# Optimization experiments

Measured on AMD Instinct MI355X. Metric: run time of the kernel, lower is better.

The kernel has to match this reference:

```python
import jax, jax.numpy as jnp
import numpy as np

B, L, A, DF = 8, 2048, 25, 128
T = 20  # amino-acid types
NUM_FUNCS = 3
D_IN = 2 * DF + T * A * 3 + 3 * (NUM_FUNCS * 4 + 1)  # 1795


def setup_inputs() -> dict:
    key = jax.random.key(0)
    ks = jax.random.split(key, 16)
    chain_emb = jax.random.normal(ks[7], (10, DF), dtype=jnp.float32)
    chain_emb = chain_emb.at[0].set(0.0)  # padding_idx=0
    return {
        'seq': jax.random.randint(ks[0], (B, L), 0, T),
        'xyz': jax.random.normal(ks[1], (B, L, A, 3), dtype=jnp.float32),
        'dihedrals': jax.random.normal(ks[2], (B, L, 3), dtype=jnp.float32),
        'chain_idx': jax.random.randint(ks[3], (B, L), 0, 10),
        'orientation': jax.random.normal(ks[4], (B, L, 3, 3), dtype=jnp.float32),
        'atom_mask': jnp.ones((B, L, A), dtype=jnp.float32),
        'aa_emb': jax.random.normal(ks[6], (T, DF), dtype=jnp.float32),
        'chain_emb': chain_emb,
        'W1': jax.random.normal(ks[8], (D_IN, 2 * DF), dtype=jnp.float32) * 0.02,
        'b1': jnp.zeros((2 * DF,), dtype=jnp.float32),
        'W2': jax.random.normal(ks[9], (2 * DF, DF), dtype=jnp.float32) * 0.05,
        'b2': jnp.zeros((DF,), dtype=jnp.float32),
        'W3': jax.random.normal(ks[10], (DF, DF), dtype=jnp.float32) * 0.05,
        'b3': jnp.zeros((DF,), dtype=jnp.float32),
        'W4': jax.random.normal(ks[11], (DF, DF), dtype=jnp.float32) * 0.05,
        'b4': jnp.zeros((DF,), dtype=jnp.float32),
    }


def _angular_encoding(x):
    # x: (..., d_in) -> (..., d_in * (num_funcs*4 + 1))
    freq = jnp.array([1.0, 2.0, 3.0, 1.0, 0.5, 1.0 / 3.0], dtype=x.dtype)
    xe = x[..., None]  # (..., d_in, 1)
    enc = jnp.concatenate([xe, jnp.sin(freq * xe), jnp.cos(freq * xe)], axis=-1)
    return enc.reshape(*x.shape[:-1], -1)


def reference(seq, xyz, dihedrals, chain_idx, orientation, atom_mask,
              aa_emb, chain_emb, W1, b1, W2, b2, W3, b3, W4, b4):
    b, l = seq.shape
    CA_IDX = 1
    aa_type_feat = aa_emb[seq]  # (b,l,DF)
    # local frame coords: R^T (x - x_CA) per atom
    xyz_rel = xyz - xyz[:, :, CA_IDX:CA_IDX + 1, :]
    xyz_local = jnp.einsum('blji,blaj->blai', orientation, xyz_rel)  # (b,l,A,3)
    # type-conditioned one-hot scatter of local coords -> (b,l,T*A*3)
    onehot = jax.nn.one_hot(seq, T, dtype=xyz.dtype)  # (b,l,T)
    coord_feat = jnp.einsum('blt,blad->bltad', onehot, xyz_local).reshape(b, l, -1)
    dihedral_feat = _angular_encoding(dihedrals)  # (b,l,39)
    chain_feat = jnp.where((chain_idx == 0)[..., None], 0.0, chain_emb[chain_idx])
    x = jnp.concatenate([aa_type_feat, coord_feat, dihedral_feat, chain_feat], axis=-1)
    h = jax.nn.relu(x @ W1 + b1)
    h = jax.nn.relu(h @ W2 + b2)
    h = jax.nn.relu(h @ W3 + b3)
    return h @ W4 + b4
```

## Files before the change

kernel.cpp:

```cpp
#include <hip/hip_runtime.h>

#define NRES   16384
#define NTYPES 20
#define CAP    1280
#define MT     32
#define CHUNKS 32
#define FPP    392
#define H1P    264
#define H2P    136


#define BUCKET_OFF  512
#define W1S_OFF     32768
#define W1C_OFF     110592
#define W2_OFF      520192
#define W3_OFF      552960
#define W4_OFF      569344

typedef __attribute__((ext_vector_type(8))) short short8;
typedef __attribute__((ext_vector_type(4))) float float4_;

__device__ __forceinline__ unsigned short f2bf(float f) {
    union { float f; unsigned int u; } v; v.f = f;
    unsigned int r = v.u + 0x7FFF + ((v.u >> 16) & 1);
    return (unsigned short)(r >> 16);
}

__global__ void zero_counts_k(int* __restrict__ cnt) {
    if (threadIdx.x < NTYPES) cnt[threadIdx.x] = 0;
}

__global__ void prep_k(const int* __restrict__ seq, int* __restrict__ cnt,
                       const float* __restrict__ W1, const float* __restrict__ W2,
                       const float* __restrict__ W3, const float* __restrict__ W4,
                       unsigned short* __restrict__ ws) {
    const int blk = blockIdx.x, tid = threadIdx.x;
    if (blk < 64) {
        __shared__ int lcnt[NTYPES], lbase[NTYPES];
        if (tid < NTYPES) lcnt[tid] = 0;
        __syncthreads();
        const int r = blk * 256 + tid;
        const int t = seq[r];
        const int sl = atomicAdd(&lcnt[t], 1);
        __syncthreads();
        if (tid < NTYPES && lcnt[tid] > 0)
            lbase[tid] = atomicAdd(&cnt[tid], lcnt[tid]);
        __syncthreads();
        const int slot = lbase[t] + sl;
        if (slot < CAP) ws[BUCKET_OFF + t * CAP + slot] = (unsigned short)r;
        return;
    }
    int i = (blk - 64) * 256 + tid;
    float v[8];
    int dst;
    if (i < 9728) {
        const int g = i >> 8, n = i & 255;
        const int s0 = g * 8;
#pragma unroll
        for (int j = 0; j < 8; ++j) {
            const int s = s0 + j;
            const int row = (s < 128) ? s : (s < 168 ? s + 1500 : s + 1499);
            v[j] = (s0 < 296) ? W1[(size_t)row * 256 + n] : 0.0f;
        }
        dst = W1S_OFF + (g * 256 + n) * 8;
    } else if ((i -= 9728) < 51200) {
        const int t = i / 2560, r2 = i - t * 2560;
        const int g = r2 >> 8, n = r2 & 255;
        const int c0 = g * 8;
#pragma unroll
        for (int j = 0; j < 8; ++j) {
            const int c = c0 + j;
            v[j] = (c < 75) ? W1[(size_t)(128 + 75 * t + c) * 256 + n] : 0.0f;
        }
        dst = W1C_OFF + ((t * 10 + g) * 256 + n) * 8;
    } else if ((i -= 51200) < 4096) {
        const int g = i >> 7, n = i & 127;
#pragma unroll
        for (int j = 0; j < 8; ++j) v[j] = W2[(size_t)(g * 8 + j) * 128 + n];
        dst = W2_OFF + (g * 128 + n) * 8;
    } else if ((i -= 4096) < 2048) {
        const int g = i >> 7, n = i & 127;
#pragma unroll
        for (int j = 0; j < 8; ++j) v[j] = W3[(size_t)(g * 8 + j) * 128 + n];
        dst = W3_OFF + (g * 128 + n) * 8;
    } else {
        i -= 2048;
        const int g = i >> 7, n = i & 127;
#pragma unroll
        for (int j = 0; j < 8; ++j) v[j] = W4[(size_t)(g * 8 + j) * 128 + n];
        dst = W4_OFF + (g * 128 + n) * 8;
    }
    short8 o;
#pragma unroll
    for (int j = 0; j < 8; ++j) o[j] = (short)f2bf(v[j]);
    *(short8*)(ws + dst) = o;
}

__global__ __launch_bounds__(512, 6) void residue_embed_k(
    const float* __restrict__ xyz, const float* __restrict__ dihedrals,
    const int* __restrict__ chain_idx, const float* __restrict__ orient,
    const float* __restrict__ aa_emb, const float* __restrict__ chain_emb,
    const float* __restrict__ b1, const float* __restrict__ b2,
    const float* __restrict__ b3, const float* __restrict__ b4,
    const unsigned short* __restrict__ ws, float* __restrict__ out)
{
    __shared__ __align__(16) unsigned short feat[MT * FPP];
    __shared__ __align__(16) unsigned short h1s[MT * H1P];
    __shared__ int ridx[MT];

    const int* cnt = (const int*)ws;
    const unsigned short* bucket = ws + BUCKET_OFF;

    const int t = blockIdx.x / CHUNKS;
    const int start = (blockIdx.x % CHUNKS) * MT;
    const int count = cnt[t];
    if (start >= count) return;
    const int mact = min(MT, count - start);
    const int tid = threadIdx.x;

    {
        const int m = tid >> 4, s = tid & 15;
        const int idx = bucket[t * CAP + min(start + m, count - 1)];
        if (s == 0) ridx[m] = idx;
        unsigned short* fm = &feat[m * FPP];
#pragma unroll
        for (int i = 0; i < 8; ++i) fm[s * 8 + i] = f2bf(aa_emb[t * 128 + s * 8 + i]);
        const int c = chain_idx[idx];
#pragma unroll
        for (int i = 0; i < 8; ++i)
            fm[248 + s * 8 + i] = f2bf((c == 0) ? 0.0f : chain_emb[c * 128 + s * 8 + i]);
        const float* xr = &xyz[(size_t)idx * 75];
        const float cax = xr[3], cay = xr[4], caz = xr[5];
        const float* R = &orient[(size_t)idx * 9];
        for (int a = s; a < 25; a += 16) {
            float rx = xr[a * 3] - cax, ry = xr[a * 3 + 1] - cay, rz = xr[a * 3 + 2] - caz;
#pragma unroll
            for (int i = 0; i < 3; ++i)
                fm[128 + a * 3 + i] = f2bf(R[i] * rx + R[3 + i] * ry + R[6 + i] * rz);
        }
        if (s < 13) {
            const int qd = (s == 0) ? 0 : (s < 7 ? s - 1 : s - 7);
            const float fq = (qd == 0) ? 1.f : (qd == 1) ? 2.f : (qd == 2) ? 3.f
                           : (qd == 3) ? 1.f : (qd == 4) ? 0.5f : (1.f / 3.f);
#pragma unroll
            for (int d = 0; d < 3; ++d) {
                float x = dihedrals[idx * 3 + d];
                float v = (s == 0) ? x : (s < 7 ? sinf(fq * x) : cosf(fq * x));
                fm[208 + d * 13 + s] = f2bf(v);
            }
        }
        if (s == 14) { for (int k = 203; k < 208; ++k) fm[k] = 0; }
        if (s == 13) fm[247] = 0;
        if (s == 12) { for (int k = 376; k < 384; ++k) fm[k] = 0; }
    }
    __syncthreads();

    const int lane = tid & 63, wv = tid >> 6;
    const int q = lane >> 4, nl = lane & 15;
    const float4_ z = {0.f, 0.f, 0.f, 0.f};

    {
        float4_ acc[2][2] = {{z, z}, {z, z}};
        const int nb = wv * 32;
#pragma unroll 2
        for (int ks = 0; ks < 12; ++ks) {
            const int kf = ks * 32 + q * 8;
            short8 a0 = *(const short8*)&feat[nl * FPP + kf];
            short8 a1 = *(const short8*)&feat[(nl + 16) * FPP + kf];
            const bool isC = (kf >= 128) && (kf < 208);
            const int g = isC ? (t * 10 + ((kf - 128) >> 3)) : (((kf < 128) ? kf : (kf - 80)) >> 3);
            const unsigned short* bp = ws + (isC ? W1C_OFF : W1S_OFF) + (size_t)g * 2048;
#pragma unroll
            for (int nt = 0; nt < 2; ++nt) {
                const int n = nb + nt * 16 + nl;
                short8 bf = *(const short8*)(bp + n * 8);
                acc[0][nt] = __builtin_amdgcn_mfma_f32_16x16x32_bf16(a0, bf, acc[0][nt], 0, 0, 0);
                acc[1][nt] = __builtin_amdgcn_mfma_f32_16x16x32_bf16(a1, bf, acc[1][nt], 0, 0, 0);
            }
        }
#pragma unroll
        for (int nt = 0; nt < 2; ++nt) {
            const int n = nb + nt * 16 + nl;
            const float bv = b1[n];
#pragma unroll
            for (int mt = 0; mt < 2; ++mt)
#pragma unroll
                for (int r = 0; r < 4; ++r)
                    h1s[(mt * 16 + q * 4 + r) * H1P + n] = f2bf(fmaxf(acc[mt][nt][r] + bv, 0.f));
        }
    }
    __syncthreads();

    unsigned short* h2s = feat;
    unsigned short* h3s = feat + MT * H2P;
    const int nb2 = wv * 16;

    {
        float4_ acc[2] = {z, z};
#pragma unroll 2
        for (int ks = 0; ks < 8; ++ks) {
            const int kf = ks * 32 + q * 8;
            short8 a0 = *(const short8*)&h1s[nl * H1P + kf];
            short8 a1 = *(const short8*)&h1s[(nl + 16) * H1P + kf];
            const int n = nb2 + nl;
            short8 bf = *(const short8*)(ws + W2_OFF + ((kf >> 3) * 128 + n) * 8);
            acc[0] = __builtin_amdgcn_mfma_f32_16x16x32_bf16(a0, bf, acc[0], 0, 0, 0);
            acc[1] = __builtin_amdgcn_mfma_f32_16x16x32_bf16(a1, bf, acc[1], 0, 0, 0);
        }
        const int n = nb2 + nl;
        const float bv = b2[n];
#pragma unroll
        for (int mt = 0; mt < 2; ++mt)
#pragma unroll
            for (int r = 0; r < 4; ++r)
                h2s[(mt * 16 + q * 4 + r) * H2P + n] = f2bf(fmaxf(acc[mt][r] + bv, 0.f));
    }
    __syncthreads();

    {
        float4_ acc[2] = {z, z};
#pragma unroll
        for (int ks = 0; ks < 4; ++ks) {
            const int kf = ks * 32 + q * 8;
            short8 a0 = *(const short8*)&h2s[nl * H2P + kf];
            short8 a1 = *(const short8*)&h2s[(nl + 16) * H2P + kf];
            const int n = nb2 + nl;
            short8 bf = *(const short8*)(ws + W3_OFF + ((kf >> 3) * 128 + n) * 8);
            acc[0] = __builtin_amdgcn_mfma_f32_16x16x32_bf16(a0, bf, acc[0], 0, 0, 0);
            acc[1] = __builtin_amdgcn_mfma_f32_16x16x32_bf16(a1, bf, acc[1], 0, 0, 0);
        }
        const int n = nb2 + nl;
        const float bv = b3[n];
#pragma unroll
        for (int mt = 0; mt < 2; ++mt)
#pragma unroll
            for (int r = 0; r < 4; ++r)
                h3s[(mt * 16 + q * 4 + r) * H2P + n] = f2bf(fmaxf(acc[mt][r] + bv, 0.f));
    }
    __syncthreads();

    {
        float4_ acc[2] = {z, z};
#pragma unroll
        for (int ks = 0; ks < 4; ++ks) {
            const int kf = ks * 32 + q * 8;
            short8 a0 = *(const short8*)&h3s[nl * H2P + kf];
            short8 a1 = *(const short8*)&h3s[(nl + 16) * H2P + kf];
            const int n = nb2 + nl;
            short8 bf = *(const short8*)(ws + W4_OFF + ((kf >> 3) * 128 + n) * 8);
            acc[0] = __builtin_amdgcn_mfma_f32_16x16x32_bf16(a0, bf, acc[0], 0, 0, 0);
            acc[1] = __builtin_amdgcn_mfma_f32_16x16x32_bf16(a1, bf, acc[1], 0, 0, 0);
        }
        const int n = nb2 + nl;
        const float bv = b4[n];
#pragma unroll
        for (int mt = 0; mt < 2; ++mt)
#pragma unroll
            for (int r = 0; r < 4; ++r) {
                const int m = mt * 16 + q * 4 + r;
                if (m < mact)
                    out[(size_t)ridx[m] * 128 + n] = acc[mt][r] + bv;
            }
    }
}

extern "C" void kernel_launch(void* const* d_in, const int* in_sizes, int n_in,
                              void* d_out, int out_size, void* d_ws, size_t ws_size,
                              hipStream_t stream) {
    const int*   seq       = (const int*)  d_in[0];
    const float* xyz       = (const float*)d_in[1];
    const float* dihedrals = (const float*)d_in[2];
    const int*   chain_idx = (const int*)  d_in[3];
    const float* orient    = (const float*)d_in[4];
    const float* aa_emb    = (const float*)d_in[6];
    const float* chain_emb = (const float*)d_in[7];
    const float* W1 = (const float*)d_in[8];
    const float* b1 = (const float*)d_in[9];
    const float* W2 = (const float*)d_in[10];
    const float* b2 = (const float*)d_in[11];
    const float* W3 = (const float*)d_in[12];
    const float* b3 = (const float*)d_in[13];
    const float* W4 = (const float*)d_in[14];
    const float* b4 = (const float*)d_in[15];

    unsigned short* wsu = (unsigned short*)d_ws;
    int* cnt = (int*)d_ws;
    float* out = (float*)d_out;

    zero_counts_k<<<1, 32, 0, stream>>>(cnt);
    prep_k<<<64 + 270, 256, 0, stream>>>(seq, cnt, W1, W2, W3, W4, wsu);
    residue_embed_k<<<NTYPES * CHUNKS, 512, 0, stream>>>(
        xyz, dihedrals, chain_idx, orient, aa_emb, chain_emb,
        b1, b2, b3, b4, wsu, out);
}
```

Before: 112.8 us.

## Precompute aa and chain embedding projections through W1 as lookup tables

The aa-type and chain embedding features are now pushed through W1 once in the prep kernel. This gives per-type and per-chain fp32 bias tables of size 20x256 and 10x256. The main kernel's first GEMM shrinks from 384 to 128 K columns, covering only coords and dihedrals, and the tables are added in the epilogue. The shared feature buffer also shrinks, and h3 now reuses h1s, which needs an extra barrier. The prep kernel gains serial 128-length dot products per output.

```diff
diff --git a/kernel.cpp b/kernel.cpp
--- a/kernel.cpp
+++ b/kernel.cpp
@@ -5,17 +5,19 @@
 #define CAP    1280
 #define MT     32
 #define CHUNKS 32
-#define FPP    392
+#define FPC    136
 #define H1P    264
 #define H2P    136
 
 
 #define BUCKET_OFF  512
 #define W1S_OFF     32768
-#define W1C_OFF     110592
-#define W2_OFF      520192
-#define W3_OFF      552960
-#define W4_OFF      569344
+#define W1C_OFF     45056
+#define W2_OFF      454656
+#define W3_OFF      487424
+#define W4_OFF      503808
+#define TB1F_OFF    260096
+#define CW1F_OFF    265216
 
 typedef __attribute__((ext_vector_type(8))) short short8;
 typedef __attribute__((ext_vector_type(4))) float float4_;
@@ -31,8 +33,10 @@
 }
 
 __global__ void prep_k(const int* __restrict__ seq, int* __restrict__ cnt,
-                       const float* __restrict__ W1, const float* __restrict__ W2,
-                       const float* __restrict__ W3, const float* __restrict__ W4,
+                       const float* __restrict__ W1, const float* __restrict__ b1,
+                       const float* __restrict__ W2, const float* __restrict__ W3,
+                       const float* __restrict__ W4, const float* __restrict__ aa_emb,
+                       const float* __restrict__ chain_emb,
                        unsigned short* __restrict__ ws) {
     const int blk = blockIdx.x, tid = threadIdx.x;
     if (blk < 64) {
@@ -51,19 +55,38 @@
         return;
     }
     int i = (blk - 64) * 256 + tid;
+    float* fws = (float*)ws;
+    if (i >= 60928) {
+        if (i < 66048) {
+            const int j = i - 60928, t = j >> 8, n = j & 255;
+            float s = b1[n];
+#pragma unroll 4
+            for (int k = 0; k < 128; ++k)
+                s = fmaf(aa_emb[t * 128 + k], W1[(size_t)k * 256 + n], s);
+            fws[TB1F_OFF + t * 256 + n] = s;
+        } else {
+            const int j = i - 66048, c = j >> 8, n = j & 255;
+            float s = 0.f;
+            if (c)
+#pragma unroll 4
+                for (int k = 0; k < 128; ++k)
+                    s = fmaf(chain_emb[c * 128 + k], W1[(size_t)(1667 + k) * 256 + n], s);
+            fws[CW1F_OFF + c * 256 + n] = s;
+        }
+        return;
+    }
     float v[8];
     int dst;
-    if (i < 9728) {
+    if (i < 1536) {
         const int g = i >> 8, n = i & 255;
         const int s0 = g * 8;
 #pragma unroll
         for (int j = 0; j < 8; ++j) {
             const int s = s0 + j;
-            const int row = (s < 128) ? s : (s < 168 ? s + 1500 : s + 1499);
-            v[j] = (s0 < 296) ? W1[(size_t)row * 256 + n] : 0.0f;
+            v[j] = (s < 39) ? W1[(size_t)(1628 + s) * 256 + n] : 0.0f;
         }
         dst = W1S_OFF + (g * 256 + n) * 8;
-    } else if ((i -= 9728) < 51200) {
+    } else if ((i -= 1536) < 51200) {
         const int t = i / 2560, r2 = i - t * 2560;
         const int g = r2 >> 8, n = r2 & 255;
         const int c0 = g * 8;
@@ -99,17 +122,17 @@
 __global__ __launch_bounds__(512, 6) void residue_embed_k(
     const float* __restrict__ xyz, const float* __restrict__ dihedrals,
     const int* __restrict__ chain_idx, const float* __restrict__ orient,
-    const float* __restrict__ aa_emb, const float* __restrict__ chain_emb,
-    const float* __restrict__ b1, const float* __restrict__ b2,
-    const float* __restrict__ b3, const float* __restrict__ b4,
+    const float* __restrict__ b2, const float* __restrict__ b3,
+    const float* __restrict__ b4,
     const unsigned short* __restrict__ ws, float* __restrict__ out)
 {
-    __shared__ __align__(16) unsigned short feat[MT * FPP];
+    __shared__ __align__(16) unsigned short feat[MT * FPC];
     __shared__ __align__(16) unsigned short h1s[MT * H1P];
-    __shared__ int ridx[MT];
+    __shared__ int ridx[MT], cidx[MT];
 
     const int* cnt = (const int*)ws;
     const unsigned short* bucket = ws + BUCKET_OFF;
+    const float* fws = (const float*)ws;
 
     const int t = blockIdx.x / CHUNKS;
     const int start = (blockIdx.x % CHUNKS) * MT;
@@ -121,14 +144,8 @@
     {
         const int m = tid >> 4, s = tid & 15;
         const int idx = bucket[t * CAP + min(start + m, count - 1)];
-        if (s == 0) ridx[m] = idx;
-        unsigned short* fm = &feat[m * FPP];
-#pragma unroll
-        for (int i = 0; i < 8; ++i) fm[s * 8 + i] = f2bf(aa_emb[t * 128 + s * 8 + i]);
-        const int c = chain_idx[idx];
-#pragma unroll
-        for (int i = 0; i < 8; ++i)
-            fm[248 + s * 8 + i] = f2bf((c == 0) ? 0.0f : chain_emb[c * 128 + s * 8 + i]);
+        if (s == 0) { ridx[m] = idx; cidx[m] = chain_idx[idx]; }
+        unsigned short* fm = &feat[m * FPC];
         const float* xr = &xyz[(size_t)idx * 75];
         const float cax = xr[3], cay = xr[4], caz = xr[5];
         const float* R = &orient[(size_t)idx * 9];
@@ -136,7 +153,7 @@
             float rx = xr[a * 3] - cax, ry = xr[a * 3 + 1] - cay, rz = xr[a * 3 + 2] - caz;
 #pragma unroll
             for (int i = 0; i < 3; ++i)
-                fm[128 + a * 3 + i] = f2bf(R[i] * rx + R[3 + i] * ry + R[6 + i] * rz);
+                fm[a * 3 + i] = f2bf(R[i] * rx + R[3 + i] * ry + R[6 + i] * rz);
         }
         if (s < 13) {
             const int qd = (s == 0) ? 0 : (s < 7 ? s - 1 : s - 7);
@@ -146,12 +163,11 @@
             for (int d = 0; d < 3; ++d) {
                 float x = dihedrals[idx * 3 + d];
                 float v = (s == 0) ? x : (s < 7 ? sinf(fq * x) : cosf(fq * x));
-                fm[208 + d * 13 + s] = f2bf(v);
+                fm[80 + d * 13 + s] = f2bf(v);
             }
         }
-        if (s == 14) { for (int k = 203; k < 208; ++k) fm[k] = 0; }
-        if (s == 13) fm[247] = 0;
-        if (s == 12) { for (int k = 376; k < 384; ++k) fm[k] = 0; }
+        if (s == 14) { for (int k = 75; k < 80; ++k) fm[k] = 0; }
+        if (s == 15) { for (int k = 119; k < 128; ++k) fm[k] = 0; }
     }
     __syncthreads();
 
@@ -162,14 +178,15 @@
     {
         float4_ acc[2][2] = {{z, z}, {z, z}};
         const int nb = wv * 32;
-#pragma unroll 2
-        for (int ks = 0; ks < 12; ++ks) {
+#pragma unroll
+        for (int ks = 0; ks < 4; ++ks) {
             const int kf = ks * 32 + q * 8;
-            short8 a0 = *(const short8*)&feat[nl * FPP + kf];
-            short8 a1 = *(const short8*)&feat[(nl + 16) * FPP + kf];
-            const bool isC = (kf >= 128) && (kf < 208);
-            const int g = isC ? (t * 10 + ((kf - 128) >> 3)) : (((kf < 128) ? kf : (kf - 80)) >> 3);
-            const unsigned short* bp = ws + (isC ? W1C_OFF : W1S_OFF) + (size_t)g * 2048;
+            short8 a0 = *(const short8*)&feat[nl * FPC + kf];
+            short8 a1 = *(const short8*)&feat[(nl + 16) * FPC + kf];
+            const int g = kf >> 3;
+            const unsigned short* bp = (g < 10)
+                ? ws + W1C_OFF + (size_t)(t * 10 + g) * 2048
+                : ws + W1S_OFF + (size_t)(g - 10) * 2048;
 #pragma unroll
             for (int nt = 0; nt < 2; ++nt) {
                 const int n = nb + nt * 16 + nl;
@@ -181,18 +198,21 @@
 #pragma unroll
         for (int nt = 0; nt < 2; ++nt) {
             const int n = nb + nt * 16 + nl;
-            const float bv = b1[n];
+            const float tb = fws[TB1F_OFF + t * 256 + n];
 #pragma unroll
             for (int mt = 0; mt < 2; ++mt)
 #pragma unroll
-                for (int r = 0; r < 4; ++r)
-                    h1s[(mt * 16 + q * 4 + r) * H1P + n] = f2bf(fmaxf(acc[mt][nt][r] + bv, 0.f));
+                for (int r = 0; r < 4; ++r) {
+                    const int m = mt * 16 + q * 4 + r;
+                    const float cw = fws[CW1F_OFF + cidx[m] * 256 + n];
+                    h1s[m * H1P + n] = f2bf(fmaxf(acc[mt][nt][r] + tb + cw, 0.f));
+                }
         }
     }
     __syncthreads();
 
     unsigned short* h2s = feat;
-    unsigned short* h3s = feat + MT * H2P;
+    unsigned short* h3s = h1s;
     const int nb2 = wv * 16;
 
     {
@@ -207,6 +227,7 @@
             acc[0] = __builtin_amdgcn_mfma_f32_16x16x32_bf16(a0, bf, acc[0], 0, 0, 0);
             acc[1] = __builtin_amdgcn_mfma_f32_16x16x32_bf16(a1, bf, acc[1], 0, 0, 0);
         }
+        __syncthreads();
         const int n = nb2 + nl;
         const float bv = b2[n];
 #pragma unroll
@@ -288,8 +309,8 @@
     float* out = (float*)d_out;
 
     zero_counts_k<<<1, 32, 0, stream>>>(cnt);
-    prep_k<<<64 + 270, 256, 0, stream>>>(seq, cnt, W1, W2, W3, W4, wsu);
+    prep_k<<<64 + 268, 256, 0, stream>>>(seq, cnt, W1, b1, W2, W3, W4,
+                                         aa_emb, chain_emb, wsu);
     residue_embed_k<<<NTYPES * CHUNKS, 512, 0, stream>>>(
-        xyz, dihedrals, chain_idx, orient, aa_emb, chain_emb,
-        b1, b2, b3, b4, wsu, out);
-}
+        xyz, dihedrals, chain_idx, orient, b2, b3, b4, wsu, out);
+}
```

Result: slower. 115.1 us (+2.1%).
